# Kernel tuning notes

Measured on AMD Instinct MI355X. Metric: run time of the kernel, lower is better.

## Reference

```python
import jax, jax.numpy as jnp
import numpy as np

DEPTH = 16                      # complete binary tree depth (root level = DEPTH)
NUM_LEVELS = DEPTH + 1          # node_order in [0, DEPTH]
N_NODES = 2 ** (DEPTH + 1) - 1  # 131071
VOCAB = 50000
EMB = 128
HID = 128


def setup_inputs() -> dict:
    key = jax.random.key(0)
    ks = jax.random.split(key, 6)
    # --- deterministic complete binary tree structure ---
    idx = np.arange(N_NODES)
    depth = np.floor(np.log2(idx + 1)).astype(np.int64)  # root idx 0 has depth 0
    node_order = (DEPTH - depth).astype(np.int64)        # leaves evaluated first (order 0)
    internal = np.arange(2 ** DEPTH - 1)                 # nodes with children
    parents = np.repeat(internal, 2)                     # consecutive grouping per parent
    children = np.stack([2 * internal + 1, 2 * internal + 2], axis=1).ravel()
    adjacency_list = np.stack([parents, children], axis=1).astype(np.int64)
    edge_order = node_order[parents]
    s = 0.02
    return {
        "features": jax.random.randint(ks[0], (N_NODES,), 0, VOCAB),
        "node_order": jnp.asarray(node_order),
        "adjacency_list": jnp.asarray(adjacency_list),
        "edge_order": jnp.asarray(edge_order),
        "emb": jax.random.normal(ks[1], (VOCAB, EMB), jnp.float32) * s,
        "W_iou": jax.random.normal(ks[2], (EMB, 3 * HID), jnp.float32) * s,
        "b_iou": jnp.zeros((3 * HID,), jnp.float32),
        "U_iou": jax.random.normal(ks[3], (HID, 3 * HID), jnp.float32) * s,
        "W_f": jax.random.normal(ks[4], (EMB, HID), jnp.float32) * s,
        "b_f": jnp.zeros((HID,), jnp.float32),
        "U_f": jax.random.normal(ks[5], (HID, HID), jnp.float32) * s,
    }


def reference(features, node_order, adjacency_list, edge_order,
              emb, W_iou, b_iou, U_iou, W_f, b_f, U_f):
    x = emb[features]                                   # [N, EMB] embedding lookup
    par = adjacency_list[:, 0]                          # [E]
    chd = adjacency_list[:, 1]                          # [E]
    Wx = x @ W_iou + b_iou                              # [N, 3H] input contributions (precomputed)
    Wfx = x @ W_f + b_f                                 # [N, H] forget-gate input term
    N = x.shape[0]
    H = W_f.shape[1]
    h = jnp.zeros((N, H), x.dtype)
    c = jnp.zeros((N, H), x.dtype)
    # level-synchronous TreeLSTM: leaves (level 0) up to root
    for lvl in range(NUM_LEVELS):
        nmask = (node_order == lvl)[:, None]            # nodes updated this level
        emask = (edge_order == lvl)[:, None].astype(x.dtype)  # edges feeding them
        child_h = h[chd]                                # [E, H] gather children
        child_c = c[chd]
        h_sum = jax.ops.segment_sum(child_h * emask, par, num_segments=N)  # [N, H]
        iou = Wx + h_sum @ U_iou                        # [N, 3H]
        i, o, u = jnp.split(iou, 3, axis=1)
        i = jax.nn.sigmoid(i)
        o = jax.nn.sigmoid(o)
        u = jnp.tanh(u)
        f = jax.nn.sigmoid(Wfx[par] + child_h @ U_f)    # [E, H] per-edge forget gate
        c_sum = jax.ops.segment_sum(f * child_c * emask, par, num_segments=N)
        c_new = i * u + c_sum                           # level 0: c_sum == 0 -> i*u (leaf branch)
        c = jnp.where(nmask, c_new, c)
        h = jnp.where(nmask, o * jnp.tanh(c_new), h)
    return h, c
```

## Files before the change

### kernel.cpp

```cpp
#include <hip/hip_runtime.h>
#include <math.h>

#define NN 131071
#define HD 128
#define N_INTERNAL 65535
#define LEAF_BASE 65535

typedef short bf16x8 __attribute__((ext_vector_type(8)));
typedef unsigned short u16x8 __attribute__((ext_vector_type(8)));
typedef unsigned short u16x4 __attribute__((ext_vector_type(4)));
typedef float f32x4 __attribute__((ext_vector_type(4)));

__device__ __forceinline__ float sigm(float z) { return 1.0f / (1.0f + __expf(-z)); }
__device__ __forceinline__ float tanh_f(float z) { return 1.0f - 2.0f / (__expf(2.0f * z) + 1.0f); }

__device__ __forceinline__ unsigned short f2bf(float f) {
    unsigned u = __float_as_uint(f);
    u += 0x7FFFu + ((u >> 16) & 1u);
    return (unsigned short)(u >> 16);
}
__device__ __forceinline__ float bf2f(unsigned short b) {
    return __uint_as_float(((unsigned)b) << 16);
}

__device__ __forceinline__ f32x4 mfma16(bf16x8 a, bf16x8 b, f32x4 c) {
    return __builtin_amdgcn_mfma_f32_16x16x32_bf16(a, b, c, 0, 0, 0);
}

__device__ __forceinline__ float4 addf4(float4 a, float4 b) {
    float4 r; r.x = a.x + b.x; r.y = a.y + b.y; r.z = a.z + b.z; r.w = a.w + b.w; return r;
}

__device__ __forceinline__ bf16x8 pk8(float4 a, float4 b) {
    u16x8 p;
    p[0] = f2bf(a.x); p[1] = f2bf(a.y); p[2] = f2bf(a.z); p[3] = f2bf(a.w);
    p[4] = f2bf(b.x); p[5] = f2bf(b.y); p[6] = f2bf(b.z); p[7] = f2bf(b.w);
    return *(bf16x8*)&p;
}

__device__ __forceinline__ bf16x8 lds_frag(const unsigned short* region, int row, int ks, int kl) {
    int cc = ks * 4 + kl;
    return *(const bf16x8*)&region[row * HD + ((cc ^ (row & 7)) << 3)];
}

__device__ __forceinline__ bf16x8 lds_frag2(const unsigned short* region, int row, int ks, int kl) {
    int cc = ks * 4 + kl;
    return *(const bf16x8*)&region[row * HD + ((cc ^ ((row >> 1) & 7)) << 3)];
}

__device__ __forceinline__ bf16x8 frag2(const unsigned short* M, int ct, int ks, int lane) {
    return *(const bf16x8*)&M[(((ct * 4 + ks) * 64) + lane) * 8];
}

__device__ __forceinline__ bf16x8 row_frag(const unsigned short* rowp, int ks, int kl) {
    return *(const bf16x8*)&rowp[ks * 32 + kl * 8];
}

__global__ __launch_bounds__(256) void build_packed(
    const float* __restrict__ W_iou, const float* __restrict__ U_iou,
    const float* __restrict__ W_f, const float* __restrict__ U_f,
    unsigned short* __restrict__ ws)
{
    int f = blockIdx.x * 256 + threadIdx.x;
    int mat = f >> 13;
    int rem = f & 8191;
    int ct = rem >> 8;
    int ks = (rem >> 6) & 3;
    int lane = rem & 63;
    int col = ct * 16 + (lane & 15);
    int k0 = ks * 32 + (lane >> 4) * 8;
    u16x8 out;
#pragma unroll
    for (int e = 0; e < 8; ++e) {
        int k = k0 + e;
        float v;
        if (mat == 0) v = (col < 384) ? W_iou[k * 384 + col] : W_f[k * HD + (col - 384)];
        else          v = (col < 384) ? U_iou[k * 384 + col] : U_f[k * HD + (col - 384)];
        out[e] = f2bf(v);
    }
    *(u16x8*)&ws[(size_t)f * 8] = out;
}

__global__ __launch_bounds__(256) void conv_emb(
    const float* __restrict__ emb, unsigned short* __restrict__ emb16)
{
    size_t idx = ((size_t)blockIdx.x * 256 + threadIdx.x) * 8;
    float4 a = *(const float4*)(emb + idx);
    float4 b = *(const float4*)(emb + idx + 4);
    bf16x8 v = pk8(a, b);
    *(bf16x8*)&emb16[idx] = v;
}

__global__ __launch_bounds__(512) void xp_leaf2(
    const int* __restrict__ feat, const unsigned short* __restrict__ emb16,
    const unsigned short* __restrict__ WT2,
    const float* __restrict__ b_iou, const float* __restrict__ b_f,
    unsigned short* __restrict__ XPb, unsigned short* __restrict__ hb16,
    float* __restrict__ hbuf, float* __restrict__ cbuf)
{
    const int t = threadIdx.x;
    const int m0 = blockIdx.x * 64;
    const int lane = t & 63, w = t >> 6;
    const int jq = w & 3, mh = w >> 2;
    const int l15 = lane & 15, kl = lane >> 4;

    int na0 = m0 + (mh * 2 + 0) * 16 + l15;
    int na1 = m0 + (mh * 2 + 1) * 16 + l15;
    const unsigned short* x0p = emb16 + (size_t)feat[na0 < NN ? na0 : NN - 1] * HD;
    const unsigned short* x1p = emb16 + (size_t)feat[na1 < NN ? na1 : NN - 1] * HD;

    f32x4 zero = {0.f, 0.f, 0.f, 0.f};
    f32x4 acc[4][2][2];
#pragma unroll
    for (int g = 0; g < 4; ++g)
#pragma unroll
        for (int mp = 0; mp < 2; ++mp)
#pragma unroll
            for (int jt = 0; jt < 2; ++jt) acc[g][mp][jt] = zero;

#pragma unroll
    for (int ks = 0; ks < 4; ++ks) {
        bf16x8 a0 = row_frag(x0p, ks, kl);
        bf16x8 a1 = row_frag(x1p, ks, kl);
#pragma unroll
        for (int g = 0; g < 4; ++g) {
#pragma unroll
            for (int jt = 0; jt < 2; ++jt) {
                bf16x8 b = frag2(WT2, g * 8 + jq * 2 + jt, ks, lane);
                acc[g][0][jt] = mfma16(a0, b, acc[g][0][jt]);
                acc[g][1][jt] = mfma16(a1, b, acc[g][1][jt]);
            }
        }
    }

#pragma unroll
    for (int mp = 0; mp < 2; ++mp) {
#pragma unroll
        for (int jt = 0; jt < 2; ++jt) {
            int j = jq * 32 + jt * 16 + l15;
            int nb = m0 + (mh * 2 + mp) * 16 + kl * 4;
            float bi = b_iou[j], bo = b_iou[HD + j], bu = b_iou[2 * HD + j], bf = b_f[j];
#pragma unroll
            for (int r = 0; r < 4; ++r) {
                int n = nb + r;
                if (n >= NN) continue;
                if (n >= LEAF_BASE) {
                    float iv = sigm(acc[0][mp][jt][r] + bi);
                    float ov = sigm(acc[1][mp][jt][r] + bo);
                    float uv = tanh_f(acc[2][mp][jt][r] + bu);
                    float cv = iv * uv;
                    float hv = ov * tanh_f(cv);
                    cbuf[(size_t)n * HD + j] = cv;
                    hbuf[(size_t)n * HD + j] = hv;
                    hb16[(size_t)n * HD + j] = f2bf(hv);
                } else {
                    u16x4 pk;
                    pk[0] = f2bf(acc[0][mp][jt][r] + bi);
                    pk[1] = f2bf(acc[1][mp][jt][r] + bo);
                    pk[2] = f2bf(acc[2][mp][jt][r] + bu);
                    pk[3] = f2bf(acc[3][mp][jt][r] + bf);
                    *(u16x4*)&XPb[((size_t)n * HD + j) * 4] = pk;
                }
            }
        }
    }
}

__global__ __launch_bounds__(512) void level_u3(
    const unsigned short* __restrict__ UT2, const unsigned short* __restrict__ XPb,
    const unsigned short* __restrict__ hb16_c, unsigned short* __restrict__ hb16,
    float* __restrict__ hbuf, float* __restrict__ cbuf, int base)
{
    __shared__ unsigned short chlds[128 * HD];
    const int t = threadIdx.x;
    const int m0 = blockIdx.x * 64;
    const size_t cr0 = 2 * (size_t)(base + m0) + 1;

    {
        int r = t >> 2, q = t & 3;
        const unsigned short* src = hb16_c + (cr0 + r) * HD + q * 32;
#pragma unroll
        for (int i = 0; i < 4; ++i) {
            bf16x8 v = *(const bf16x8*)(src + i * 8);
            int cc = q * 4 + i;
            *(bf16x8*)&chlds[r * HD + ((cc ^ ((r >> 1) & 7)) << 3)] = v;
        }
    }
    __syncthreads();

    const int lane = t & 63, w = t >> 6;
    const int jq = w & 3, mh = w >> 2;
    const int l15 = lane & 15, kl = lane >> 4;

    f32x4 zero = {0.f, 0.f, 0.f, 0.f};
    f32x4 acc[5][2][2];
#pragma unroll
    for (int g = 0; g < 5; ++g)
#pragma unroll
        for (int mp = 0; mp < 2; ++mp)
#pragma unroll
            for (int jt = 0; jt < 2; ++jt) acc[g][mp][jt] = zero;

#pragma unroll
    for (int ks = 0; ks < 4; ++ks) {
        bf16x8 ah1[2], ah2[2];
#pragma unroll
        for (int mp = 0; mp < 2; ++mp) {
            int pr = mh * 32 + mp * 16 + l15;
            ah1[mp] = lds_frag2(chlds, 2 * pr + 0, ks, kl);
            ah2[mp] = lds_frag2(chlds, 2 * pr + 1, ks, kl);
        }
#pragma unroll
        for (int jt = 0; jt < 2; ++jt) {
            bf16x8 Bi = frag2(UT2,  0 + jq * 2 + jt, ks, lane);
            bf16x8 Bo = frag2(UT2,  8 + jq * 2 + jt, ks, lane);
            bf16x8 Bu = frag2(UT2, 16 + jq * 2 + jt, ks, lane);
            bf16x8 Bf = frag2(UT2, 24 + jq * 2 + jt, ks, lane);
#pragma unroll
            for (int mp = 0; mp < 2; ++mp) {
                acc[0][mp][jt] = mfma16(ah1[mp], Bi, mfma16(ah2[mp], Bi, acc[0][mp][jt]));
                acc[1][mp][jt] = mfma16(ah1[mp], Bo, mfma16(ah2[mp], Bo, acc[1][mp][jt]));
                acc[2][mp][jt] = mfma16(ah1[mp], Bu, mfma16(ah2[mp], Bu, acc[2][mp][jt]));
                acc[3][mp][jt] = mfma16(ah1[mp], Bf, acc[3][mp][jt]);
                acc[4][mp][jt] = mfma16(ah2[mp], Bf, acc[4][mp][jt]);
            }
        }
    }

#pragma unroll
    for (int mp = 0; mp < 2; ++mp) {
#pragma unroll
        for (int jt = 0; jt < 2; ++jt) {
            int j = jq * 32 + jt * 16 + l15;
#pragma unroll
            for (int r = 0; r < 4; ++r) {
                int n = base + m0 + (mh * 2 + mp) * 16 + kl * 4 + r;
                u16x4 pk = *(const u16x4*)&XPb[((size_t)n * HD + j) * 4];
                float iv = sigm(acc[0][mp][jt][r] + bf2f(pk[0]));
                float ov = sigm(acc[1][mp][jt][r] + bf2f(pk[1]));
                float uv = tanh_f(acc[2][mp][jt][r] + bf2f(pk[2]));
                float fx = bf2f(pk[3]);
                float f1 = sigm(acc[3][mp][jt][r] + fx);
                float f2 = sigm(acc[4][mp][jt][r] + fx);
                float c1 = cbuf[(size_t)(2 * n + 1) * HD + j];
                float c2 = cbuf[(size_t)(2 * n + 2) * HD + j];
                float cn = fmaf(iv, uv, fmaf(f1, c1, f2 * c2));
                float hn = ov * tanh_f(cn);
                cbuf[(size_t)n * HD + j] = cn;
                hbuf[(size_t)n * HD + j] = hn;
                hb16[(size_t)n * HD + j] = f2bf(hn);
            }
        }
    }
}

__global__ __launch_bounds__(512) void tail_kernel3(
    const unsigned short* __restrict__ UT2, const unsigned short* __restrict__ XPb,
    float* __restrict__ hbuf, float* __restrict__ cbuf)
{
    __shared__ unsigned short hlds[255 * HD];
    const int t = threadIdx.x;

    {
        int n = 127 + (t >> 2);
        int c0 = (t & 3) * 32;
        const float* src = hbuf + (size_t)n * HD + c0;
#pragma unroll
        for (int q = 0; q < 4; ++q) {
            float4 a = *(const float4*)(src + q * 8);
            float4 b = *(const float4*)(src + q * 8 + 4);
            int cc = (c0 >> 3) + q;
            bf16x8 v = pk8(a, b);
            *(bf16x8*)&hlds[n * HD + ((cc ^ (n & 7)) << 3)] = v;
        }
    }
    __syncthreads();

    const int lane = t & 63, w = t >> 6;
    const int jq = w & 3, mh = w >> 2;
    const int l15 = lane & 15, kl = lane >> 4;

#pragma unroll 1
    for (int lvl = 10; lvl <= 16; ++lvl) {
        const int count = 1 << (16 - lvl);
        const int base = count - 1;
        if (mh * 32 < count) {
            f32x4 zero = {0.f, 0.f, 0.f, 0.f};
            f32x4 acc[5][2][2];
#pragma unroll
            for (int g = 0; g < 5; ++g)
#pragma unroll
                for (int mp = 0; mp < 2; ++mp)
#pragma unroll
                    for (int jt = 0; jt < 2; ++jt) acc[g][mp][jt] = zero;

#pragma unroll
            for (int ks = 0; ks < 4; ++ks) {
                bf16x8 ah1[2], ah2[2];
#pragma unroll
                for (int mp = 0; mp < 2; ++mp) {
                    int row = mh * 32 + mp * 16 + l15;
                    int rr = row < count ? row : count - 1;
                    int n = base + rr;
                    ah1[mp] = lds_frag(hlds, 2 * n + 1, ks, kl);
                    ah2[mp] = lds_frag(hlds, 2 * n + 2, ks, kl);
                }
#pragma unroll
                for (int jt = 0; jt < 2; ++jt) {
                    bf16x8 Bi = frag2(UT2,  0 + jq * 2 + jt, ks, lane);
                    bf16x8 Bo = frag2(UT2,  8 + jq * 2 + jt, ks, lane);
                    bf16x8 Bu = frag2(UT2, 16 + jq * 2 + jt, ks, lane);
                    bf16x8 Bf = frag2(UT2, 24 + jq * 2 + jt, ks, lane);
#pragma unroll
                    for (int mp = 0; mp < 2; ++mp) {
                        acc[0][mp][jt] = mfma16(ah1[mp], Bi, mfma16(ah2[mp], Bi, acc[0][mp][jt]));
                        acc[1][mp][jt] = mfma16(ah1[mp], Bo, mfma16(ah2[mp], Bo, acc[1][mp][jt]));
                        acc[2][mp][jt] = mfma16(ah1[mp], Bu, mfma16(ah2[mp], Bu, acc[2][mp][jt]));
                        acc[3][mp][jt] = mfma16(ah1[mp], Bf, acc[3][mp][jt]);
                        acc[4][mp][jt] = mfma16(ah2[mp], Bf, acc[4][mp][jt]);
                    }
                }
            }

#pragma unroll
            for (int mp = 0; mp < 2; ++mp) {
#pragma unroll
                for (int jt = 0; jt < 2; ++jt) {
                    int j = jq * 32 + jt * 16 + l15;
#pragma unroll
                    for (int r = 0; r < 4; ++r) {
                        int row = mh * 32 + mp * 16 + kl * 4 + r;
                        if (row >= count) continue;
                        int n = base + row;
                        u16x4 pk = *(const u16x4*)&XPb[((size_t)n * HD + j) * 4];
                        float iv = sigm(acc[0][mp][jt][r] + bf2f(pk[0]));
                        float ov = sigm(acc[1][mp][jt][r] + bf2f(pk[1]));
                        float uv = tanh_f(acc[2][mp][jt][r] + bf2f(pk[2]));
                        float fx = bf2f(pk[3]);
                        float f1 = sigm(acc[3][mp][jt][r] + fx);
                        float f2 = sigm(acc[4][mp][jt][r] + fx);
                        float c1 = cbuf[(size_t)(2 * n + 1) * HD + j];
                        float c2 = cbuf[(size_t)(2 * n + 2) * HD + j];
                        float cn = fmaf(iv, uv, fmaf(f1, c1, f2 * c2));
                        float hn = ov * tanh_f(cn);
                        cbuf[(size_t)n * HD + j] = cn;
                        hbuf[(size_t)n * HD + j] = hn;
                        int cc = j >> 3;
                        hlds[n * HD + ((cc ^ (n & 7)) << 3) + (j & 7)] = f2bf(hn);
                    }
                }
            }
        }
        __syncthreads();
    }
}

template <int MT>
__global__ __launch_bounds__(128) void leaf_kernel(
    const int* __restrict__ feat, const float* __restrict__ emb,
    const float* __restrict__ W_iou, const float* __restrict__ b_iou,
    float* __restrict__ hbuf, float* __restrict__ cbuf, int base)
{
    __shared__ float X[MT][HD];
    const int j = threadIdx.x;
    const int m0 = blockIdx.x * MT;
#pragma unroll
    for (int m = 0; m < MT; ++m) {
        int n = base + m0 + m;
        X[m][j] = emb[(size_t)feat[n] * HD + j];
    }
    __syncthreads();
    float ai[MT], ao[MT], au[MT];
#pragma unroll
    for (int m = 0; m < MT; ++m) {
        ai[m] = b_iou[j]; ao[m] = b_iou[HD + j]; au[m] = b_iou[2 * HD + j];
    }
#pragma unroll 4
    for (int k = 0; k < HD; ++k) {
        float wi = W_iou[k * 3 * HD + j];
        float wo = W_iou[k * 3 * HD + HD + j];
        float wu = W_iou[k * 3 * HD + 2 * HD + j];
#pragma unroll
        for (int m = 0; m < MT; ++m) {
            float x = X[m][k];
            ai[m] = fmaf(x, wi, ai[m]); ao[m] = fmaf(x, wo, ao[m]); au[m] = fmaf(x, wu, au[m]);
        }
    }
#pragma unroll
    for (int m = 0; m < MT; ++m) {
        int n = base + m0 + m;
        float iv = sigm(ai[m]); float ov = sigm(ao[m]); float uv = tanh_f(au[m]);
        float cv = iv * uv;
        cbuf[(size_t)n * HD + j] = cv;
        hbuf[(size_t)n * HD + j] = ov * tanh_f(cv);
    }
}

template <int MT>
__global__ __launch_bounds__(128) void level_kernel(
    const int* __restrict__ feat, const float* __restrict__ emb,
    const float* __restrict__ W_iou, const float* __restrict__ b_iou,
    const float* __restrict__ U_iou,
    const float* __restrict__ W_f, const float* __restrict__ b_f,
    const float* __restrict__ U_f,
    float* __restrict__ hbuf, float* __restrict__ cbuf, int base)
{
    __shared__ float X[MT][HD];
    __shared__ float H1[MT][HD];
    __shared__ float H2[MT][HD];
    const int j = threadIdx.x;
    const int m0 = blockIdx.x * MT;
#pragma unroll
    for (int m = 0; m < MT; ++m) {
        int n = base + m0 + m;
        X[m][j]  = emb[(size_t)feat[n] * HD + j];
        H1[m][j] = hbuf[(size_t)(2 * n + 1) * HD + j];
        H2[m][j] = hbuf[(size_t)(2 * n + 2) * HD + j];
    }
    __syncthreads();
    float ai[MT], ao[MT], au[MT], g1[MT], g2[MT];
#pragma unroll
    for (int m = 0; m < MT; ++m) {
        ai[m] = b_iou[j]; ao[m] = b_iou[HD + j]; au[m] = b_iou[2 * HD + j];
        g1[m] = b_f[j]; g2[m] = b_f[j];
    }
#pragma unroll 2
    for (int k = 0; k < HD; ++k) {
        float wi = W_iou[k * 3 * HD + j];
        float wo = W_iou[k * 3 * HD + HD + j];
        float wu = W_iou[k * 3 * HD + 2 * HD + j];
        float ui = U_iou[k * 3 * HD + j];
        float uo = U_iou[k * 3 * HD + HD + j];
        float uu = U_iou[k * 3 * HD + 2 * HD + j];
        float wf = W_f[k * HD + j];
        float uf = U_f[k * HD + j];
#pragma unroll
        for (int m = 0; m < MT; ++m) {
            float x = X[m][k]; float h1 = H1[m][k]; float h2 = H2[m][k]; float hs = h1 + h2;
            ai[m] = fmaf(x, wi, fmaf(hs, ui, ai[m]));
            ao[m] = fmaf(x, wo, fmaf(hs, uo, ao[m]));
            au[m] = fmaf(x, wu, fmaf(hs, uu, au[m]));
            g1[m] = fmaf(x, wf, fmaf(h1, uf, g1[m]));
            g2[m] = fmaf(x, wf, fmaf(h2, uf, g2[m]));
        }
    }
#pragma unroll
    for (int m = 0; m < MT; ++m) {
        int n = base + m0 + m;
        float iv = sigm(ai[m]); float ov = sigm(ao[m]); float uv = tanh_f(au[m]);
        float f1 = sigm(g1[m]); float f2 = sigm(g2[m]);
        float c1 = cbuf[(size_t)(2 * n + 1) * HD + j];
        float c2 = cbuf[(size_t)(2 * n + 2) * HD + j];
        float cn = fmaf(iv, uv, fmaf(f1, c1, f2 * c2));
        cbuf[(size_t)n * HD + j] = cn;
        hbuf[(size_t)n * HD + j] = ov * tanh_f(cn);
    }
}

extern "C" void kernel_launch(void* const* d_in, const int* in_sizes, int n_in,
                              void* d_out, int out_size, void* d_ws, size_t ws_size,
                              hipStream_t stream)
{
    const int*   feat  = (const int*)d_in[0];
    const float* emb   = (const float*)d_in[4];
    const float* W_iou = (const float*)d_in[5];
    const float* b_iou = (const float*)d_in[6];
    const float* U_iou = (const float*)d_in[7];
    const float* W_f   = (const float*)d_in[8];
    const float* b_f   = (const float*)d_in[9];
    const float* U_f   = (const float*)d_in[10];

    float* hbuf = (float*)d_out;
    float* cbuf = hbuf + (size_t)NN * HD;

    const size_t PACK_BYTES = 2u * 65536u * 2u;
    const size_t XP_BYTES   = (size_t)N_INTERNAL * HD * 4 * 2;
    const size_t HB_BYTES   = (size_t)131072 * HD * 2;
    const size_t EMB_BYTES  = (size_t)50000 * HD * 2;
    if (ws_size >= PACK_BYTES + XP_BYTES + HB_BYTES + EMB_BYTES) {
        unsigned short* wpk = (unsigned short*)d_ws;
        const unsigned short* WT2 = wpk;
        const unsigned short* UT2 = wpk + 65536;
        unsigned short* XPb  = (unsigned short*)((char*)d_ws + PACK_BYTES);
        unsigned short* hb16 = (unsigned short*)((char*)d_ws + PACK_BYTES + XP_BYTES);
        unsigned short* emb16= (unsigned short*)((char*)d_ws + PACK_BYTES + XP_BYTES + HB_BYTES);

        build_packed<<<64, 256, 0, stream>>>(W_iou, U_iou, W_f, U_f, wpk);
        conv_emb<<<3125, 256, 0, stream>>>(emb, emb16);

        xp_leaf2<<<2048, 512, 0, stream>>>(feat, emb16, WT2, b_iou, b_f, XPb, hb16, hbuf, cbuf);

        for (int lvl = 1; lvl <= 9; ++lvl) {
            const int count = 1 << (16 - lvl);
            const int base  = count - 1;
            level_u3<<<count / 64, 512, 0, stream>>>(UT2, XPb, hb16, hb16, hbuf, cbuf, base);
        }
        tail_kernel3<<<1, 512, 0, stream>>>(UT2, XPb, hbuf, cbuf);
    } else {
        leaf_kernel<16><<<65536 / 16, 128, 0, stream>>>(feat, emb, W_iou, b_iou, hbuf, cbuf, 65535);
        for (int lvl = 1; lvl <= 16; ++lvl) {
            const int d = 16 - lvl;
            const int count = 1 << d;
            const int base = count - 1;
            if (count >= 16) {
                level_kernel<16><<<count / 16, 128, 0, stream>>>(
                    feat, emb, W_iou, b_iou, U_iou, W_f, b_f, U_f, hbuf, cbuf, base);
            } else if (count == 8) {
                level_kernel<8><<<1, 128, 0, stream>>>(
                    feat, emb, W_iou, b_iou, U_iou, W_f, b_f, U_f, hbuf, cbuf, base);
            } else if (count == 4) {
                level_kernel<4><<<1, 128, 0, stream>>>(
                    feat, emb, W_iou, b_iou, U_iou, W_f, b_f, U_f, hbuf, cbuf, base);
            } else if (count == 2) {
                level_kernel<2><<<1, 128, 0, stream>>>(
                    feat, emb, W_iou, b_iou, U_iou, W_f, b_f, U_f, hbuf, cbuf, base);
            } else {
                level_kernel<1><<<1, 128, 0, stream>>>(
                    feat, emb, W_iou, b_iou, U_iou, W_f, b_f, U_f, hbuf, cbuf, base);
            }
        }
    }
}
```

Baseline: 311.8 us.

## Fuse pairs of tree levels into one kernel and merge prep kernels

Adds a pair_kernel that processes two consecutive tree levels per block. The intermediate-level h values stay in LDS as bf16 and feed the next level's MFMA step directly, so they are not written to and re-read from global memory, and the number of level launches drops from nine to five. The weight-packing and embedding-conversion kernels are merged into one launch. In exchange, each block does twice the MFMA work on fewer blocks at the narrower levels, which lowers parallelism, and it still reads the child c values from global memory.

After: 374.1 us. 20.0% more time.

```diff
diff --git a/kernel.cpp b/kernel.cpp
--- a/kernel.cpp
+++ b/kernel.cpp
@@ -25,10 +25,6 @@
 
 __device__ __forceinline__ f32x4 mfma16(bf16x8 a, bf16x8 b, f32x4 c) {
     return __builtin_amdgcn_mfma_f32_16x16x32_bf16(a, b, c, 0, 0, 0);
-}
-
-__device__ __forceinline__ float4 addf4(float4 a, float4 b) {
-    float4 r; r.x = a.x + b.x; r.y = a.y + b.y; r.z = a.z + b.z; r.w = a.w + b.w; return r;
 }
 
 __device__ __forceinline__ bf16x8 pk8(float4 a, float4 b) {
@@ -56,39 +52,39 @@
     return *(const bf16x8*)&rowp[ks * 32 + kl * 8];
 }
 
-__global__ __launch_bounds__(256) void build_packed(
+__global__ __launch_bounds__(256) void prep_kernel(
     const float* __restrict__ W_iou, const float* __restrict__ U_iou,
     const float* __restrict__ W_f, const float* __restrict__ U_f,
-    unsigned short* __restrict__ ws)
-{
-    int f = blockIdx.x * 256 + threadIdx.x;
-    int mat = f >> 13;
-    int rem = f & 8191;
-    int ct = rem >> 8;
-    int ks = (rem >> 6) & 3;
-    int lane = rem & 63;
-    int col = ct * 16 + (lane & 15);
-    int k0 = ks * 32 + (lane >> 4) * 8;
-    u16x8 out;
-#pragma unroll
-    for (int e = 0; e < 8; ++e) {
-        int k = k0 + e;
-        float v;
-        if (mat == 0) v = (col < 384) ? W_iou[k * 384 + col] : W_f[k * HD + (col - 384)];
-        else          v = (col < 384) ? U_iou[k * 384 + col] : U_f[k * HD + (col - 384)];
-        out[e] = f2bf(v);
-    }
-    *(u16x8*)&ws[(size_t)f * 8] = out;
-}
-
-__global__ __launch_bounds__(256) void conv_emb(
-    const float* __restrict__ emb, unsigned short* __restrict__ emb16)
-{
-    size_t idx = ((size_t)blockIdx.x * 256 + threadIdx.x) * 8;
-    float4 a = *(const float4*)(emb + idx);
-    float4 b = *(const float4*)(emb + idx + 4);
-    bf16x8 v = pk8(a, b);
-    *(bf16x8*)&emb16[idx] = v;
+    const float* __restrict__ emb,
+    unsigned short* __restrict__ wpk, unsigned short* __restrict__ emb16)
+{
+    int bid = blockIdx.x;
+    if (bid < 3125) {
+        size_t idx = ((size_t)bid * 256 + threadIdx.x) * 8;
+        float4 a = *(const float4*)(emb + idx);
+        float4 b = *(const float4*)(emb + idx + 4);
+        bf16x8 v = pk8(a, b);
+        *(bf16x8*)&emb16[idx] = v;
+    } else {
+        int f = (bid - 3125) * 256 + threadIdx.x;
+        int mat = f >> 13;
+        int rem = f & 8191;
+        int ct = rem >> 8;
+        int ks = (rem >> 6) & 3;
+        int lane = rem & 63;
+        int col = ct * 16 + (lane & 15);
+        int k0 = ks * 32 + (lane >> 4) * 8;
+        u16x8 out;
+#pragma unroll
+        for (int e = 0; e < 8; ++e) {
+            int k = k0 + e;
+            float v;
+            if (mat == 0) v = (col < 384) ? W_iou[k * 384 + col] : W_f[k * HD + (col - 384)];
+            else          v = (col < 384) ? U_iou[k * 384 + col] : U_f[k * HD + (col - 384)];
+            out[e] = f2bf(v);
+        }
+        *(u16x8*)&wpk[(size_t)f * 8] = out;
+    }
 }
 
 __global__ __launch_bounds__(512) void xp_leaf2(
@@ -160,6 +156,182 @@
                     pk[2] = f2bf(acc[2][mp][jt][r] + bu);
                     pk[3] = f2bf(acc[3][mp][jt][r] + bf);
                     *(u16x4*)&XPb[((size_t)n * HD + j) * 4] = pk;
+                }
+            }
+        }
+    }
+}
+
+__global__ __launch_bounds__(512) void pair_kernel(
+    const unsigned short* __restrict__ UT2, const unsigned short* __restrict__ XPb,
+    unsigned short* __restrict__ hb16,
+    float* __restrict__ hbuf, float* __restrict__ cbuf, int base2)
+{
+    __shared__ unsigned short lds[256 * HD];
+    const int t = threadIdx.x;
+    const int P0 = base2 + blockIdx.x * 64;
+    const size_t g0 = 4 * (size_t)P0 + 3;
+    const int m0g = 2 * P0 + 1;
+
+    {
+        int r = t >> 1, q = t & 1;
+        const unsigned short* src = hb16 + (g0 + r) * HD + q * 64;
+#pragma unroll
+        for (int i = 0; i < 8; ++i) {
+            bf16x8 v = *(const bf16x8*)(src + i * 8);
+            int cc = q * 8 + i;
+            *(bf16x8*)&lds[r * HD + ((cc ^ ((r >> 1) & 7)) << 3)] = v;
+        }
+    }
+    __syncthreads();
+
+    const int lane = t & 63, w = t >> 6;
+    const int jq = w & 3, mh = w >> 2;
+    const int l15 = lane & 15, kl = lane >> 4;
+    f32x4 zero = {0.f, 0.f, 0.f, 0.f};
+
+    float hA[2][16];
+#pragma unroll
+    for (int half = 0; half < 2; ++half) {
+        f32x4 acc[5][2][2];
+#pragma unroll
+        for (int g = 0; g < 5; ++g)
+#pragma unroll
+            for (int mp = 0; mp < 2; ++mp)
+#pragma unroll
+                for (int jt = 0; jt < 2; ++jt) acc[g][mp][jt] = zero;
+
+#pragma unroll
+        for (int ks = 0; ks < 4; ++ks) {
+            bf16x8 ah1[2], ah2[2];
+#pragma unroll
+            for (int mp = 0; mp < 2; ++mp) {
+                int i = half * 64 + mh * 32 + mp * 16 + l15;
+                ah1[mp] = lds_frag2(lds, 2 * i + 0, ks, kl);
+                ah2[mp] = lds_frag2(lds, 2 * i + 1, ks, kl);
+            }
+#pragma unroll
+            for (int jt = 0; jt < 2; ++jt) {
+                bf16x8 Bi = frag2(UT2,  0 + jq * 2 + jt, ks, lane);
+                bf16x8 Bo = frag2(UT2,  8 + jq * 2 + jt, ks, lane);
+                bf16x8 Bu = frag2(UT2, 16 + jq * 2 + jt, ks, lane);
+                bf16x8 Bf = frag2(UT2, 24 + jq * 2 + jt, ks, lane);
+#pragma unroll
+                for (int mp = 0; mp < 2; ++mp) {
+                    acc[0][mp][jt] = mfma16(ah1[mp], Bi, mfma16(ah2[mp], Bi, acc[0][mp][jt]));
+                    acc[1][mp][jt] = mfma16(ah1[mp], Bo, mfma16(ah2[mp], Bo, acc[1][mp][jt]));
+                    acc[2][mp][jt] = mfma16(ah1[mp], Bu, mfma16(ah2[mp], Bu, acc[2][mp][jt]));
+                    acc[3][mp][jt] = mfma16(ah1[mp], Bf, acc[3][mp][jt]);
+                    acc[4][mp][jt] = mfma16(ah2[mp], Bf, acc[4][mp][jt]);
+                }
+            }
+        }
+
+#pragma unroll
+        for (int mp = 0; mp < 2; ++mp) {
+#pragma unroll
+            for (int jt = 0; jt < 2; ++jt) {
+                int j = jq * 32 + jt * 16 + l15;
+#pragma unroll
+                for (int r = 0; r < 4; ++r) {
+                    int i = half * 64 + mh * 32 + mp * 16 + kl * 4 + r;
+                    int m = m0g + i;
+                    u16x4 pk = *(const u16x4*)&XPb[((size_t)m * HD + j) * 4];
+                    float iv = sigm(acc[0][mp][jt][r] + bf2f(pk[0]));
+                    float ov = sigm(acc[1][mp][jt][r] + bf2f(pk[1]));
+                    float uv = tanh_f(acc[2][mp][jt][r] + bf2f(pk[2]));
+                    float fx = bf2f(pk[3]);
+                    float f1 = sigm(acc[3][mp][jt][r] + fx);
+                    float f2 = sigm(acc[4][mp][jt][r] + fx);
+                    float c1 = cbuf[(size_t)(2 * m + 1) * HD + j];
+                    float c2 = cbuf[(size_t)(2 * m + 2) * HD + j];
+                    float cn = fmaf(iv, uv, fmaf(f1, c1, f2 * c2));
+                    float hn = ov * tanh_f(cn);
+                    cbuf[(size_t)m * HD + j] = cn;
+                    hbuf[(size_t)m * HD + j] = hn;
+                    hA[half][mp * 8 + jt * 4 + r] = hn;
+                }
+            }
+        }
+    }
+    __syncthreads();
+
+    {
+#pragma unroll
+        for (int half = 0; half < 2; ++half)
+#pragma unroll
+            for (int mp = 0; mp < 2; ++mp)
+#pragma unroll
+                for (int jt = 0; jt < 2; ++jt) {
+                    int j = jq * 32 + jt * 16 + l15;
+                    int cc = j >> 3;
+#pragma unroll
+                    for (int r = 0; r < 4; ++r) {
+                        int i = half * 64 + mh * 32 + mp * 16 + kl * 4 + r;
+                        lds[i * HD + ((cc ^ ((i >> 1) & 7)) << 3) + (j & 7)] =
+                            f2bf(hA[half][mp * 8 + jt * 4 + r]);
+                    }
+                }
+    }
+    __syncthreads();
+
+    {
+        f32x4 acc[5][2][2];
+#pragma unroll
+        for (int g = 0; g < 5; ++g)
+#pragma unroll
+            for (int mp = 0; mp < 2; ++mp)
+#pragma unroll
+                for (int jt = 0; jt < 2; ++jt) acc[g][mp][jt] = zero;
+
+#pragma unroll
+        for (int ks = 0; ks < 4; ++ks) {
+            bf16x8 ah1[2], ah2[2];
+#pragma unroll
+            for (int mp = 0; mp < 2; ++mp) {
+                int p = mh * 32 + mp * 16 + l15;
+                ah1[mp] = lds_frag2(lds, 2 * p + 0, ks, kl);
+                ah2[mp] = lds_frag2(lds, 2 * p + 1, ks, kl);
+            }
+#pragma unroll
+            for (int jt = 0; jt < 2; ++jt) {
+                bf16x8 Bi = frag2(UT2,  0 + jq * 2 + jt, ks, lane);
+                bf16x8 Bo = frag2(UT2,  8 + jq * 2 + jt, ks, lane);
+                bf16x8 Bu = frag2(UT2, 16 + jq * 2 + jt, ks, lane);
+                bf16x8 Bf = frag2(UT2, 24 + jq * 2 + jt, ks, lane);
+#pragma unroll
+                for (int mp = 0; mp < 2; ++mp) {
+                    acc[0][mp][jt] = mfma16(ah1[mp], Bi, mfma16(ah2[mp], Bi, acc[0][mp][jt]));
+                    acc[1][mp][jt] = mfma16(ah1[mp], Bo, mfma16(ah2[mp], Bo, acc[1][mp][jt]));
+                    acc[2][mp][jt] = mfma16(ah1[mp], Bu, mfma16(ah2[mp], Bu, acc[2][mp][jt]));
+                    acc[3][mp][jt] = mfma16(ah1[mp], Bf, acc[3][mp][jt]);
+                    acc[4][mp][jt] = mfma16(ah2[mp], Bf, acc[4][mp][jt]);
+                }
+            }
+        }
+
+#pragma unroll
+        for (int mp = 0; mp < 2; ++mp) {
+#pragma unroll
+            for (int jt = 0; jt < 2; ++jt) {
+                int j = jq * 32 + jt * 16 + l15;
+#pragma unroll
+                for (int r = 0; r < 4; ++r) {
+                    int n = P0 + mh * 32 + mp * 16 + kl * 4 + r;
+                    u16x4 pk = *(const u16x4*)&XPb[((size_t)n * HD + j) * 4];
+                    float iv = sigm(acc[0][mp][jt][r] + bf2f(pk[0]));
+                    float ov = sigm(acc[1][mp][jt][r] + bf2f(pk[1]));
+                    float uv = tanh_f(acc[2][mp][jt][r] + bf2f(pk[2]));
+                    float fx = bf2f(pk[3]);
+                    float f1 = sigm(acc[3][mp][jt][r] + fx);
+                    float f2 = sigm(acc[4][mp][jt][r] + fx);
+                    float c1 = cbuf[(size_t)(2 * n + 1) * HD + j];
+                    float c2 = cbuf[(size_t)(2 * n + 2) * HD + j];
+                    float cn = fmaf(iv, uv, fmaf(f1, c1, f2 * c2));
+                    float hn = ov * tanh_f(cn);
+                    cbuf[(size_t)n * HD + j] = cn;
+                    hbuf[(size_t)n * HD + j] = hn;
+                    hb16[(size_t)n * HD + j] = f2bf(hn);
                 }
             }
         }
@@ -485,16 +657,15 @@
         unsigned short* hb16 = (unsigned short*)((char*)d_ws + PACK_BYTES + XP_BYTES);
         unsigned short* emb16= (unsigned short*)((char*)d_ws + PACK_BYTES + XP_BYTES + HB_BYTES);
 
-        build_packed<<<64, 256, 0, stream>>>(W_iou, U_iou, W_f, U_f, wpk);
-        conv_emb<<<3125, 256, 0, stream>>>(emb, emb16);
-
+        prep_kernel<<<3189, 256, 0, stream>>>(W_iou, U_iou, W_f, U_f, emb, wpk, emb16);
         xp_leaf2<<<2048, 512, 0, stream>>>(feat, emb16, WT2, b_iou, b_f, XPb, hb16, hbuf, cbuf);
 
-        for (int lvl = 1; lvl <= 9; ++lvl) {
-            const int count = 1 << (16 - lvl);
-            const int base  = count - 1;
-            level_u3<<<count / 64, 512, 0, stream>>>(UT2, XPb, hb16, hb16, hbuf, cbuf, base);
-        }
+        pair_kernel<<<256, 512, 0, stream>>>(UT2, XPb, hb16, hbuf, cbuf, 16383);
+        pair_kernel<<<64, 512, 0, stream>>>(UT2, XPb, hb16, hbuf, cbuf, 4095);
+        pair_kernel<<<16, 512, 0, stream>>>(UT2, XPb, hb16, hbuf, cbuf, 1023);
+        pair_kernel<<<4, 512, 0, stream>>>(UT2, XPb, hb16, hbuf, cbuf, 255);
+
+        level_u3<<<2, 512, 0, stream>>>(UT2, XPb, hb16, hb16, hbuf, cbuf, 127);
         tail_kernel3<<<1, 512, 0, stream>>>(UT2, XPb, hbuf, cbuf);
     } else {
         leaf_kernel<16><<<65536 / 16, 128, 0, stream>>>(feat, emb, W_iou, b_iou, hbuf, cbuf, 65535);
```
